# Optimization experiments

Measured on AMD Instinct MI355X. Metric: run time of the kernel, lower is better.

The kernel has to match this reference:

```python
import jax, jax.numpy as jnp
import numpy as np

N_NODES = 80000
N_EDGES = 1280000
N_FEAT = 4
HIDDEN = 64
N_CLASSES = 2
N_GRAPHS = 64
BN_EPS = 1e-5


def setup_inputs() -> dict:
    key = jax.random.key(0)
    ks = jax.random.split(key, 16)
    x = jax.random.normal(ks[0], (N_NODES, N_FEAT), dtype=jnp.float32)
    edge_index = jax.random.randint(ks[1], (2, N_EDGES), 0, N_NODES, dtype=jnp.int64)
    batch = jnp.sort(jax.random.randint(ks[2], (N_NODES,), 0, N_GRAPHS, dtype=jnp.int64))

    def lin_w(k, fan_in, fan_out):
        bound = 1.0 / np.sqrt(fan_in)
        return jax.random.uniform(k, (fan_in, fan_out), jnp.float32, -bound, bound)

    inp = {
        "x": x, "edge_index": edge_index, "batch": batch,
        # BatchNorm1d (eval mode: running stats)
        "bn_gamma": jnp.ones((N_FEAT,), jnp.float32),
        "bn_beta": jnp.zeros((N_FEAT,), jnp.float32),
        "bn_mean": jnp.zeros((N_FEAT,), jnp.float32),
        "bn_var": jnp.ones((N_FEAT,), jnp.float32),
        # GraphConv layers: out = agg @ W_rel + b_rel + x @ W_root
        "W1_rel": lin_w(ks[3], N_FEAT, HIDDEN), "b1_rel": jnp.zeros((HIDDEN,), jnp.float32),
        "W1_root": lin_w(ks[4], N_FEAT, HIDDEN),
        "W2_rel": lin_w(ks[5], HIDDEN, HIDDEN), "b2_rel": jnp.zeros((HIDDEN,), jnp.float32),
        "W2_root": lin_w(ks[6], HIDDEN, HIDDEN),
        "W3_rel": lin_w(ks[7], HIDDEN, HIDDEN), "b3_rel": jnp.zeros((HIDDEN,), jnp.float32),
        "W3_root": lin_w(ks[8], HIDDEN, HIDDEN),
        "lin_W": lin_w(ks[9], HIDDEN, N_CLASSES),
        "lin_b": jnp.zeros((N_CLASSES,), jnp.float32),
    }
    return inp


def _graph_conv(x, src, dst, W_rel, b_rel, W_root):
    # PyG GraphConv: x_i' = W_root x_i + W_rel * sum_{j in N(i)} x_j + b_rel
    agg = jax.ops.segment_sum(x[src], dst, num_segments=N_NODES)  # [N, C_in]
    return agg @ W_rel + b_rel + x @ W_root


def reference(x, edge_index, batch,
              bn_gamma, bn_beta, bn_mean, bn_var,
              W1_rel, b1_rel, W1_root,
              W2_rel, b2_rel, W2_root,
              W3_rel, b3_rel, W3_root,
              lin_W, lin_b):
    src, dst = edge_index[0], edge_index[1]
    # BatchNorm1d, eval mode (running stats); dropout is a no-op in eval.
    h = (x - bn_mean) * (bn_gamma * jax.lax.rsqrt(bn_var + BN_EPS)) + bn_beta
    h = jax.nn.relu(_graph_conv(h, src, dst, W1_rel, b1_rel, W1_root))
    h = jax.nn.relu(_graph_conv(h, src, dst, W2_rel, b2_rel, W2_root))
    h = _graph_conv(h, src, dst, W3_rel, b3_rel, W3_root)
    # global mean pool over graphs
    sums = jax.ops.segment_sum(h, batch, num_segments=N_GRAPHS)        # [G, H]
    cnts = jax.ops.segment_sum(jnp.ones((h.shape[0],), h.dtype), batch,
                               num_segments=N_GRAPHS)                  # [G]
    pooled = sums / jnp.maximum(cnts, 1.0)[:, None]
    return pooled @ lin_W + lin_b  # [G, num_classes]
```

## Files before the change

kernel.cpp:

```cpp
#include <hip/hip_runtime.h>
#include <hip/hip_bf16.h>

#define N_NODES 80000
#define N_EDGES 1280000
#define N_FEAT 4
#define HIDDEN 64
#define N_GRAPHS 64
#define BN_EPS 1e-5f

#define NBUCK 313
#define BCAP 8000

typedef unsigned short ushort_t;
typedef __attribute__((ext_vector_type(8))) short bf16x8;
typedef __attribute__((ext_vector_type(4))) float f32x4;

__device__ __forceinline__ float bf2f(ushort_t v) {
    return __uint_as_float(((unsigned)v) << 16);
}
__device__ __forceinline__ ushort_t f2bf(float f) {
    unsigned u = __float_as_uint(f);
    u += 0x7FFFu + ((u >> 16) & 1u);
    return (ushort_t)(u >> 16);
}

__global__ void wprep_kernel(const float* __restrict__ W2_rel,
                             const float* __restrict__ W2_root,
                             const float* __restrict__ W3_rel,
                             const float* __restrict__ W3_root,
                             ushort_t* __restrict__ WcatT2,
                             ushort_t* __restrict__ WcatT3,
                             int* __restrict__ bcursor,
                             float* __restrict__ pool,
                             float* __restrict__ cnt) {
    int i = blockIdx.x * blockDim.x + threadIdx.x;
    int which = i >= 64 * 128;
    int j = i & (64 * 128 - 1);
    int n = j >> 7, k = j & 127;
    const float* Wr = which ? W3_rel : W2_rel;
    const float* Wo = which ? W3_root : W2_root;
    ushort_t* Wc = which ? WcatT3 : WcatT2;
    float w = (k < 64) ? Wr[k * 64 + n] : Wo[(k - 64) * 64 + n];
    Wc[j] = f2bf(w);
    if (i < 4096) pool[i] = 0.f;
    else if (i < 4160) cnt[i - 4096] = 0.f;
    else if (i < 4160 + NBUCK) bcursor[i - 4160] = 0;
}

__global__ __launch_bounds__(256) void bucket_kernel(
        const int* __restrict__ src, const int* __restrict__ dst,
        unsigned* __restrict__ pairs, int* __restrict__ bcursor) {
    __shared__ int hist[NBUCK];
    __shared__ int base[NBUCK];
    for (int i = threadIdx.x; i < NBUCK; i += 256) hist[i] = 0;
    __syncthreads();
    int d[16], r[16];
#pragma unroll
    for (int g = 0; g < 4; ++g) {
        int e = blockIdx.x * 4096 + g * 1024 + threadIdx.x * 4;
        if (e + 4 <= N_EDGES) {
            int4 dd = *(const int4*)&dst[e];
            d[g * 4 + 0] = dd.x; d[g * 4 + 1] = dd.y;
            d[g * 4 + 2] = dd.z; d[g * 4 + 3] = dd.w;
            r[g * 4 + 0] = atomicAdd(&hist[dd.x >> 8], 1);
            r[g * 4 + 1] = atomicAdd(&hist[dd.y >> 8], 1);
            r[g * 4 + 2] = atomicAdd(&hist[dd.z >> 8], 1);
            r[g * 4 + 3] = atomicAdd(&hist[dd.w >> 8], 1);
        } else {
            d[g * 4] = -1;
        }
    }
    __syncthreads();
    for (int i = threadIdx.x; i < NBUCK; i += 256) {
        int c = hist[i];
        base[i] = c ? atomicAdd(&bcursor[i], c) : 0;
    }
    __syncthreads();
#pragma unroll
    for (int g = 0; g < 4; ++g) {
        int e = blockIdx.x * 4096 + g * 1024 + threadIdx.x * 4;
        if (e + 4 <= N_EDGES) {
            int4 ss = *(const int4*)&src[e];
            int sv[4] = {ss.x, ss.y, ss.z, ss.w};
#pragma unroll
            for (int k = 0; k < 4; ++k) {
                int dk = d[g * 4 + k];
                int b = dk >> 8;
                int pos = base[b] + r[g * 4 + k];
                if (pos < BCAP)
                    pairs[(size_t)b * BCAP + pos] =
                        (unsigned)sv[k] | (((unsigned)dk & 255u) << 17);
            }
        }
    }
}

__global__ __launch_bounds__(256) void csr_build_kernel(
        const unsigned* __restrict__ pairs, const int* __restrict__ bcursor,
        int* __restrict__ rowstart, int* __restrict__ csr) {
    __shared__ int degl[256];
    __shared__ int pref[256];
    __shared__ int curs[256];
    const int b = blockIdx.x;
    const int t = threadIdx.x;
    int partial = 0;
    for (int i = t; i < b; i += 256) partial += min(bcursor[i], BCAP);
    pref[t] = partial;
    __syncthreads();
    for (int off = 128; off > 0; off >>= 1) {
        if (t < off) pref[t] += pref[t + off];
        __syncthreads();
    }
    const int base = pref[0];
    const int cntb = min(bcursor[b], BCAP);
    __syncthreads();
    degl[t] = 0;
    __syncthreads();
    const unsigned* pb = pairs + (size_t)b * BCAP;
    for (int i = t * 4; i < cntb; i += 1024) {
        if (i + 4 <= cntb) {
            uint4 p4 = *(const uint4*)&pb[i];
            atomicAdd(&degl[p4.x >> 17], 1);
            atomicAdd(&degl[p4.y >> 17], 1);
            atomicAdd(&degl[p4.z >> 17], 1);
            atomicAdd(&degl[p4.w >> 17], 1);
        } else {
            for (int k = i; k < cntb; ++k) atomicAdd(&degl[pb[k] >> 17], 1);
        }
    }
    __syncthreads();
    int v = degl[t];
    pref[t] = v;
    __syncthreads();
    for (int off = 1; off < 256; off <<= 1) {
        int u = (t >= off) ? pref[t - off] : 0;
        __syncthreads();
        pref[t] += u;
        __syncthreads();
    }
    int excl = pref[t] - v;
    int node = b * 256 + t;
    if (node < N_NODES) rowstart[node] = base + excl;
    if (b == NBUCK - 1 && t == 255) rowstart[N_NODES] = base + cntb;
    curs[t] = excl;
    __syncthreads();
    for (int i = t * 4; i < cntb; i += 1024) {
        if (i + 4 <= cntb) {
            uint4 p4 = *(const uint4*)&pb[i];
            unsigned pv[4] = {p4.x, p4.y, p4.z, p4.w};
#pragma unroll
            for (int k = 0; k < 4; ++k) {
                int pos = atomicAdd(&curs[pv[k] >> 17], 1);
                csr[base + pos] = (int)(pv[k] & 0x1FFFFu);
            }
        } else {
            for (int k = i; k < cntb; ++k) {
                unsigned p = pb[k];
                int pos = atomicAdd(&curs[p >> 17], 1);
                csr[base + pos] = (int)(p & 0x1FFFFu);
            }
        }
    }
}

__global__ __launch_bounds__(256) void layer1_kernel(
        const float* __restrict__ x, ushort_t* __restrict__ h1,
        const int* __restrict__ rowstart, const int* __restrict__ csr,
        const float* __restrict__ Wrel, const float* __restrict__ Wroot,
        const float* __restrict__ b,
        const float* __restrict__ gamma, const float* __restrict__ beta,
        const float* __restrict__ mean, const float* __restrict__ var) {
    const int lane = threadIdx.x & 63;
    const int wid = threadIdx.x >> 6;
    float scale[4], shift[4];
#pragma unroll
    for (int k = 0; k < 4; ++k) {
        float sc = gamma[k] * rsqrtf(var[k] + BN_EPS);
        scale[k] = sc;
        shift[k] = beta[k] - mean[k] * sc;
    }
    float wrel2[4], wroot2[4];
    float crel = 0.f, croot = 0.f;
#pragma unroll
    for (int k = 0; k < 4; ++k) {
        float wr = Wrel[k * 64 + lane], wo = Wroot[k * 64 + lane];
        wrel2[k] = scale[k] * wr;  crel += shift[k] * wr;
        wroot2[k] = scale[k] * wo; croot += shift[k] * wo;
    }
    const float bj = b[lane] + croot;
    const int slot = lane >> 2;
    const int f = lane & 3;
    const int node = __builtin_amdgcn_readfirstlane(blockIdx.x * 4 + wid);
    const int e0 = rowstart[node], e1 = rowstart[node + 1];
    const float deg = (float)(e1 - e0);
    const int last = e1 - 1;
    float part = 0.f;
    for (int e = e0; e < e1; e += 16) {
        int s = csr[min(e + slot, last)];
        float v = x[s * 4 + f];
        part += (e + slot < e1) ? v : 0.f;
    }
    part += __shfl_xor(part, 4);
    part += __shfl_xor(part, 8);
    part += __shfl_xor(part, 16);
    part += __shfl_xor(part, 32);
    float a0 = __shfl(part, 0), a1 = __shfl(part, 1);
    float a2 = __shfl(part, 2), a3 = __shfl(part, 3);
    float x0 = x[node * 4 + 0], x1 = x[node * 4 + 1];
    float x2 = x[node * 4 + 2], x3 = x[node * 4 + 3];
    float out = bj + deg * crel
              + a0 * wrel2[0] + a1 * wrel2[1] + a2 * wrel2[2] + a3 * wrel2[3]
              + x0 * wroot2[0] + x1 * wroot2[1] + x2 * wroot2[2] + x3 * wroot2[3];
    h1[(size_t)node * 64 + lane] = f2bf(fmaxf(out, 0.f));
}

__global__ __launch_bounds__(256) void gather_kernel(
        const ushort_t* __restrict__ hin, ushort_t* __restrict__ Gagg,
        const int* __restrict__ rowstart, const int* __restrict__ csr) {
    const int lane = threadIdx.x & 63;
    const int l4 = lane & 15;
    const int q = lane >> 4;
    const int node = __builtin_amdgcn_readfirstlane(blockIdx.x * 4 + (threadIdx.x >> 6));
    const int e0 = rowstart[node], e1 = rowstart[node + 1];
    float ax[4], ay[4], az[4], aw[4];
#pragma unroll
    for (int j = 0; j < 4; ++j) { ax[j] = 0.f; ay[j] = 0.f; az[j] = 0.f; aw[j] = 0.f; }
    int e = e0;
    for (; e + 16 <= e1; e += 16) {
        int idx = csr[e + (lane & 15)];
#pragma unroll
        for (int j = 0; j < 4; ++j) {
            int s = __shfl(idx, 4 * j + q);
            uint2 rp = *(const uint2*)&hin[(size_t)s * 64 + 4 * l4];
            ax[j] += __uint_as_float(rp.x << 16);
            ay[j] += __uint_as_float(rp.x & 0xFFFF0000u);
            az[j] += __uint_as_float(rp.y << 16);
            aw[j] += __uint_as_float(rp.y & 0xFFFF0000u);
        }
    }
    if (e < e1) {
        const int rem = e1 - e;
        const int last = e1 - 1;
        int idx = csr[min(e + (lane & 15), last)];
#pragma unroll
        for (int j = 0; j < 4; ++j) {
            int slot = 4 * j + q;
            int s = __shfl(idx, slot);
            uint2 rp = *(const uint2*)&hin[(size_t)s * 64 + 4 * l4];
            bool ok = slot < rem;
            ax[j] += ok ? __uint_as_float(rp.x << 16) : 0.f;
            ay[j] += ok ? __uint_as_float(rp.x & 0xFFFF0000u) : 0.f;
            az[j] += ok ? __uint_as_float(rp.y << 16) : 0.f;
            aw[j] += ok ? __uint_as_float(rp.y & 0xFFFF0000u) : 0.f;
        }
    }
    float fx = (ax[0] + ax[1]) + (ax[2] + ax[3]);
    float fy = (ay[0] + ay[1]) + (ay[2] + ay[3]);
    float fz = (az[0] + az[1]) + (az[2] + az[3]);
    float fw = (aw[0] + aw[1]) + (aw[2] + aw[3]);
    fx += __shfl_xor(fx, 16); fx += __shfl_xor(fx, 32);
    fy += __shfl_xor(fy, 16); fy += __shfl_xor(fy, 32);
    fz += __shfl_xor(fz, 16); fz += __shfl_xor(fz, 32);
    fw += __shfl_xor(fw, 16); fw += __shfl_xor(fw, 32);
    if (q == 0) {
        uint2 ap;
        ap.x = (unsigned)f2bf(fx) | ((unsigned)f2bf(fy) << 16);
        ap.y = (unsigned)f2bf(fz) | ((unsigned)f2bf(fw) << 16);
        ((uint2*)(Gagg + (size_t)node * 64))[l4] = ap;
    }
}

__global__ __launch_bounds__(256) void gemm_kernel(
        const ushort_t* __restrict__ Gagg, const ushort_t* __restrict__ hin,
        ushort_t* __restrict__ hout,
        const ushort_t* __restrict__ WcatT, const float* __restrict__ b,
        int relu) {
    const int lane = threadIdx.x & 63;
    const int col = lane & 15;
    const int grp = lane >> 4;

    bf16x8 bf[4][4];
#pragma unroll
    for (int kt = 0; kt < 4; ++kt)
#pragma unroll
        for (int nt = 0; nt < 4; ++nt)
            bf[kt][nt] = *(const bf16x8*)&WcatT[(nt * 16 + col) * 128 + kt * 32 + grp * 8];

    float bj[4];
#pragma unroll
    for (int nt = 0; nt < 4; ++nt) bj[nt] = b[nt * 16 + col];

    const int tile = blockIdx.x * 4 + (threadIdx.x >> 6);
    if (tile >= N_NODES / 16) return;
    const int node0 = tile * 16;

    const ushort_t* ga = Gagg + (size_t)(node0 + col) * 64 + grp * 8;
    const ushort_t* ha = hin + (size_t)(node0 + col) * 64 + grp * 8;
    f32x4 acc0 = {0.f, 0.f, 0.f, 0.f};
    f32x4 acc1 = {0.f, 0.f, 0.f, 0.f};
    f32x4 acc2 = {0.f, 0.f, 0.f, 0.f};
    f32x4 acc3 = {0.f, 0.f, 0.f, 0.f};
#pragma unroll
    for (int kt = 0; kt < 4; ++kt) {
        bf16x8 a = (kt < 2) ? *(const bf16x8*)(ga + kt * 32)
                            : *(const bf16x8*)(ha + (kt - 2) * 32);
        acc0 = __builtin_amdgcn_mfma_f32_16x16x32_bf16(a, bf[kt][0], acc0, 0, 0, 0);
        acc1 = __builtin_amdgcn_mfma_f32_16x16x32_bf16(a, bf[kt][1], acc1, 0, 0, 0);
        acc2 = __builtin_amdgcn_mfma_f32_16x16x32_bf16(a, bf[kt][2], acc2, 0, 0, 0);
        acc3 = __builtin_amdgcn_mfma_f32_16x16x32_bf16(a, bf[kt][3], acc3, 0, 0, 0);
    }

#pragma unroll
    for (int nt = 0; nt < 4; ++nt) {
        f32x4 acc = (nt == 0) ? acc0 : (nt == 1) ? acc1 : (nt == 2) ? acc2 : acc3;
        const int c = nt * 16 + col;
#pragma unroll
        for (int r = 0; r < 4; ++r) {
            int row = grp * 4 + r;
            float v = acc[r] + bj[nt];
            if (relu) v = fmaxf(v, 0.f);
            hout[(size_t)(node0 + row) * 64 + c] = f2bf(v);
        }
    }
}

__global__ void pool_kernel(const ushort_t* __restrict__ h3, const int* __restrict__ batch,
                            float* __restrict__ pool, float* __restrict__ cnt) {
    const int lane = threadIdx.x & 63;
    const int gw = (blockIdx.x * blockDim.x + threadIdx.x) >> 6;
    const int nW = (gridDim.x * blockDim.x) >> 6;
    const int chunk = (N_NODES + nW - 1) / nW;
    int n0 = gw * chunk;
    int n1 = n0 + chunk; if (n1 > N_NODES) n1 = N_NODES;
    if (n0 >= N_NODES) return;
    float acc = 0.f;
    int cur = batch[n0];
    int cl = 0;
#define POOL_FLUSH() do { atomicAdd(&pool[cur * 64 + lane], acc); \
        if (lane == 0) atomicAdd(&cnt[cur], (float)cl); acc = 0.f; cl = 0; } while (0)
    int n = n0;
    for (; n + 8 <= n1; n += 8) {
        float v0 = bf2f(h3[(size_t)(n + 0) * 64 + lane]);
        float v1 = bf2f(h3[(size_t)(n + 1) * 64 + lane]);
        float v2 = bf2f(h3[(size_t)(n + 2) * 64 + lane]);
        float v3 = bf2f(h3[(size_t)(n + 3) * 64 + lane]);
        float v4 = bf2f(h3[(size_t)(n + 4) * 64 + lane]);
        float v5 = bf2f(h3[(size_t)(n + 5) * 64 + lane]);
        float v6 = bf2f(h3[(size_t)(n + 6) * 64 + lane]);
        float v7 = bf2f(h3[(size_t)(n + 7) * 64 + lane]);
        int g0 = batch[n + 0], g1 = batch[n + 1], g2 = batch[n + 2], g3 = batch[n + 3];
        int g4 = batch[n + 4], g5 = batch[n + 5], g6 = batch[n + 6], g7 = batch[n + 7];
        if (g0 != cur) { POOL_FLUSH(); cur = g0; } acc += v0; cl++;
        if (g1 != cur) { POOL_FLUSH(); cur = g1; } acc += v1; cl++;
        if (g2 != cur) { POOL_FLUSH(); cur = g2; } acc += v2; cl++;
        if (g3 != cur) { POOL_FLUSH(); cur = g3; } acc += v3; cl++;
        if (g4 != cur) { POOL_FLUSH(); cur = g4; } acc += v4; cl++;
        if (g5 != cur) { POOL_FLUSH(); cur = g5; } acc += v5; cl++;
        if (g6 != cur) { POOL_FLUSH(); cur = g6; } acc += v6; cl++;
        if (g7 != cur) { POOL_FLUSH(); cur = g7; } acc += v7; cl++;
    }
    for (; n < n1; ++n) {
        int g = batch[n];
        if (g != cur) { POOL_FLUSH(); cur = g; }
        acc += bf2f(h3[(size_t)n * 64 + lane]);
        cl++;
    }
    atomicAdd(&pool[cur * 64 + lane], acc);
    if (lane == 0) atomicAdd(&cnt[cur], (float)cl);
#undef POOL_FLUSH
}

__global__ void head_kernel(const float* __restrict__ pool, const float* __restrict__ cnt,
                            const float* __restrict__ linW, const float* __restrict__ linb,
                            float* __restrict__ out) {
    int g = threadIdx.x >> 1;
    int c = threadIdx.x & 1;
    if (g < N_GRAPHS) {
        float inv = 1.0f / fmaxf(cnt[g], 1.0f);
        float acc = linb[c];
        for (int j = 0; j < 64; ++j) acc += pool[g * 64 + j] * inv * linW[j * 2 + c];
        out[g * 2 + c] = acc;
    }
}

extern "C" void kernel_launch(void* const* d_in, const int* in_sizes, int n_in,
                              void* d_out, int out_size, void* d_ws, size_t ws_size,
                              hipStream_t stream) {
    const float* x = (const float*)d_in[0];
    const int* edge_index = (const int*)d_in[1];
    const int* batch = (const int*)d_in[2];
    const float* bn_gamma = (const float*)d_in[3];
    const float* bn_beta = (const float*)d_in[4];
    const float* bn_mean = (const float*)d_in[5];
    const float* bn_var = (const float*)d_in[6];
    const float* W1_rel = (const float*)d_in[7];
    const float* b1_rel = (const float*)d_in[8];
    const float* W1_root = (const float*)d_in[9];
    const float* W2_rel = (const float*)d_in[10];
    const float* b2_rel = (const float*)d_in[11];
    const float* W2_root = (const float*)d_in[12];
    const float* W3_rel = (const float*)d_in[13];
    const float* b3_rel = (const float*)d_in[14];
    const float* W3_root = (const float*)d_in[15];
    const float* lin_W = (const float*)d_in[16];
    const float* lin_b = (const float*)d_in[17];
    float* out = (float*)d_out;

    const int* e_src = edge_index;
    const int* e_dst = edge_index + N_EDGES;

    ushort_t* h1 = (ushort_t*)d_ws;
    ushort_t* h2 = h1 + 5120000;
    float* pool = (float*)(h2 + 5120000);
    float* cnt = pool + 4096;
    int* bcursor = (int*)(cnt + 64);
    int* rowstart = bcursor + 640;
    int* csr = rowstart + 80016;
    ushort_t* WcatT2 = (ushort_t*)(csr + 1280000);
    ushort_t* WcatT3 = WcatT2 + 8192;
    ushort_t* Gagg = (ushort_t*)(WcatT3 + 8192 + 16);
    unsigned* pairs = (unsigned*)h1;
    ushort_t* h3 = h1;

    wprep_kernel<<<64, 256, 0, stream>>>(W2_rel, W2_root, W3_rel, W3_root,
                                         WcatT2, WcatT3, bcursor, pool, cnt);

    bucket_kernel<<<(N_EDGES + 4095) / 4096, 256, 0, stream>>>(
        e_src, e_dst, pairs, bcursor);
    csr_build_kernel<<<NBUCK, 256, 0, stream>>>(pairs, bcursor, rowstart, csr);

    layer1_kernel<<<N_NODES / 4, 256, 0, stream>>>(x, h1, rowstart, csr, W1_rel, W1_root,
                                                   b1_rel, bn_gamma, bn_beta, bn_mean, bn_var);

    gather_kernel<<<N_NODES / 4, 256, 0, stream>>>(h1, Gagg, rowstart, csr);
    gemm_kernel<<<N_NODES / 64, 256, 0, stream>>>(Gagg, h1, h2, WcatT2, b2_rel, 1);

    gather_kernel<<<N_NODES / 4, 256, 0, stream>>>(h2, Gagg, rowstart, csr);
    gemm_kernel<<<N_NODES / 64, 256, 0, stream>>>(Gagg, h2, h3, WcatT3, b3_rel, 0);

    pool_kernel<<<256, 256, 0, stream>>>(h3, batch, pool, cnt);
    head_kernel<<<1, 128, 0, stream>>>(pool, cnt, lin_W, lin_b, out);
}
```

Baseline: 173.3 us.

## Fuse neighbor gather with MFMA GEMM per layer and make layer1 grid-stride

Merges the gather and GEMM kernels into one kernel per GraphConv layer. Each block aggregates 16 nodes into a shared-memory tile, then each of its four waves computes one 16-column slice with MFMA, so the Gagg intermediate no longer makes a round trip through global memory. Layer1 becomes a persistent grid-stride kernel with 1024-thread blocks and loses its masked tail handling. In exchange, each block waits on a barrier behind its slowest node, and fewer gather waves run per tile.

```diff
diff --git a/kernel.cpp b/kernel.cpp
--- a/kernel.cpp
+++ b/kernel.cpp
@@ -163,7 +163,7 @@
     }
 }
 
-__global__ __launch_bounds__(256) void layer1_kernel(
+__global__ __launch_bounds__(1024) void layer1_kernel(
         const float* __restrict__ x, ushort_t* __restrict__ h1,
         const int* __restrict__ rowstart, const int* __restrict__ csr,
         const float* __restrict__ Wrel, const float* __restrict__ Wroot,
@@ -188,139 +188,121 @@
         wroot2[k] = scale[k] * wo; croot += shift[k] * wo;
     }
     const float bj = b[lane] + croot;
-    const int slot = lane >> 2;
+    const int sub = lane >> 2;
     const int f = lane & 3;
-    const int node = __builtin_amdgcn_readfirstlane(blockIdx.x * 4 + wid);
-    const int e0 = rowstart[node], e1 = rowstart[node + 1];
-    const float deg = (float)(e1 - e0);
-    const int last = e1 - 1;
-    float part = 0.f;
-    for (int e = e0; e < e1; e += 16) {
-        int s = csr[min(e + slot, last)];
-        float v = x[s * 4 + f];
-        part += (e + slot < e1) ? v : 0.f;
-    }
-    part += __shfl_xor(part, 4);
-    part += __shfl_xor(part, 8);
-    part += __shfl_xor(part, 16);
-    part += __shfl_xor(part, 32);
-    float a0 = __shfl(part, 0), a1 = __shfl(part, 1);
-    float a2 = __shfl(part, 2), a3 = __shfl(part, 3);
-    float x0 = x[node * 4 + 0], x1 = x[node * 4 + 1];
-    float x2 = x[node * 4 + 2], x3 = x[node * 4 + 3];
-    float out = bj + deg * crel
-              + a0 * wrel2[0] + a1 * wrel2[1] + a2 * wrel2[2] + a3 * wrel2[3]
-              + x0 * wroot2[0] + x1 * wroot2[1] + x2 * wroot2[2] + x3 * wroot2[3];
-    h1[(size_t)node * 64 + lane] = f2bf(fmaxf(out, 0.f));
-}
-
-__global__ __launch_bounds__(256) void gather_kernel(
-        const ushort_t* __restrict__ hin, ushort_t* __restrict__ Gagg,
-        const int* __restrict__ rowstart, const int* __restrict__ csr) {
+    const int nW = gridDim.x * 16;
+    for (int n0 = blockIdx.x * 16 + wid; n0 < N_NODES; n0 += nW) {
+        const int node = __builtin_amdgcn_readfirstlane(n0);
+        const int e0 = rowstart[node], e1 = rowstart[node + 1];
+        const float deg = (float)(e1 - e0);
+        float part = 0.f;
+        for (int e = e0 + sub; e < e1; e += 16) {
+            int s = csr[e];
+            part += x[s * 4 + f];
+        }
+        part += __shfl_xor(part, 4);
+        part += __shfl_xor(part, 8);
+        part += __shfl_xor(part, 16);
+        part += __shfl_xor(part, 32);
+        float a0 = __shfl(part, 0), a1 = __shfl(part, 1);
+        float a2 = __shfl(part, 2), a3 = __shfl(part, 3);
+        float x0 = x[node * 4 + 0], x1 = x[node * 4 + 1];
+        float x2 = x[node * 4 + 2], x3 = x[node * 4 + 3];
+        float out = bj + deg * crel
+                  + a0 * wrel2[0] + a1 * wrel2[1] + a2 * wrel2[2] + a3 * wrel2[3]
+                  + x0 * wroot2[0] + x1 * wroot2[1] + x2 * wroot2[2] + x3 * wroot2[3];
+        h1[(size_t)node * 64 + lane] = f2bf(fmaxf(out, 0.f));
+    }
+}
+
+__global__ __launch_bounds__(256) void fused_layer_kernel(
+        const ushort_t* __restrict__ hin, ushort_t* __restrict__ hout,
+        const int* __restrict__ rowstart, const int* __restrict__ csr,
+        const ushort_t* __restrict__ WcatT, const float* __restrict__ b,
+        int relu) {
+    __shared__ ushort_t As[16][72];
     const int lane = threadIdx.x & 63;
+    const int wid = threadIdx.x >> 6;
     const int l4 = lane & 15;
     const int q = lane >> 4;
-    const int node = __builtin_amdgcn_readfirstlane(blockIdx.x * 4 + (threadIdx.x >> 6));
-    const int e0 = rowstart[node], e1 = rowstart[node + 1];
-    float ax[4], ay[4], az[4], aw[4];
-#pragma unroll
-    for (int j = 0; j < 4; ++j) { ax[j] = 0.f; ay[j] = 0.f; az[j] = 0.f; aw[j] = 0.f; }
-    int e = e0;
-    for (; e + 16 <= e1; e += 16) {
-        int idx = csr[e + (lane & 15)];
-#pragma unroll
-        for (int j = 0; j < 4; ++j) {
-            int s = __shfl(idx, 4 * j + q);
-            uint2 rp = *(const uint2*)&hin[(size_t)s * 64 + 4 * l4];
-            ax[j] += __uint_as_float(rp.x << 16);
-            ay[j] += __uint_as_float(rp.x & 0xFFFF0000u);
-            az[j] += __uint_as_float(rp.y << 16);
-            aw[j] += __uint_as_float(rp.y & 0xFFFF0000u);
-        }
-    }
-    if (e < e1) {
-        const int rem = e1 - e;
-        const int last = e1 - 1;
-        int idx = csr[min(e + (lane & 15), last)];
-#pragma unroll
-        for (int j = 0; j < 4; ++j) {
-            int slot = 4 * j + q;
-            int s = __shfl(idx, slot);
-            uint2 rp = *(const uint2*)&hin[(size_t)s * 64 + 4 * l4];
-            bool ok = slot < rem;
-            ax[j] += ok ? __uint_as_float(rp.x << 16) : 0.f;
-            ay[j] += ok ? __uint_as_float(rp.x & 0xFFFF0000u) : 0.f;
-            az[j] += ok ? __uint_as_float(rp.y << 16) : 0.f;
-            aw[j] += ok ? __uint_as_float(rp.y & 0xFFFF0000u) : 0.f;
-        }
-    }
-    float fx = (ax[0] + ax[1]) + (ax[2] + ax[3]);
-    float fy = (ay[0] + ay[1]) + (ay[2] + ay[3]);
-    float fz = (az[0] + az[1]) + (az[2] + az[3]);
-    float fw = (aw[0] + aw[1]) + (aw[2] + aw[3]);
-    fx += __shfl_xor(fx, 16); fx += __shfl_xor(fx, 32);
-    fy += __shfl_xor(fy, 16); fy += __shfl_xor(fy, 32);
-    fz += __shfl_xor(fz, 16); fz += __shfl_xor(fz, 32);
-    fw += __shfl_xor(fw, 16); fw += __shfl_xor(fw, 32);
-    if (q == 0) {
-        uint2 ap;
-        ap.x = (unsigned)f2bf(fx) | ((unsigned)f2bf(fy) << 16);
-        ap.y = (unsigned)f2bf(fz) | ((unsigned)f2bf(fw) << 16);
-        ((uint2*)(Gagg + (size_t)node * 64))[l4] = ap;
-    }
-}
-
-__global__ __launch_bounds__(256) void gemm_kernel(
-        const ushort_t* __restrict__ Gagg, const ushort_t* __restrict__ hin,
-        ushort_t* __restrict__ hout,
-        const ushort_t* __restrict__ WcatT, const float* __restrict__ b,
-        int relu) {
-    const int lane = threadIdx.x & 63;
+    const int node0 = blockIdx.x * 16;
+
+    for (int i = 0; i < 4; ++i) {
+        const int row = wid * 4 + i;
+        const int node = __builtin_amdgcn_readfirstlane(node0 + row);
+        const int e0 = rowstart[node], e1 = rowstart[node + 1];
+        float ax[4], ay[4], az[4], aw[4];
+#pragma unroll
+        for (int j = 0; j < 4; ++j) { ax[j] = 0.f; ay[j] = 0.f; az[j] = 0.f; aw[j] = 0.f; }
+        int e = e0;
+        for (; e + 16 <= e1; e += 16) {
+            int idx = csr[e + (lane & 15)];
+#pragma unroll
+            for (int j = 0; j < 4; ++j) {
+                int s = __shfl(idx, 4 * j + q);
+                uint2 rp = *(const uint2*)&hin[(size_t)s * 64 + 4 * l4];
+                ax[j] += __uint_as_float(rp.x << 16);
+                ay[j] += __uint_as_float(rp.x & 0xFFFF0000u);
+                az[j] += __uint_as_float(rp.y << 16);
+                aw[j] += __uint_as_float(rp.y & 0xFFFF0000u);
+            }
+        }
+        if (e < e1) {
+            const int rem = e1 - e;
+            const int last = e1 - 1;
+            int idx = csr[min(e + (lane & 15), last)];
+#pragma unroll
+            for (int j = 0; j < 4; ++j) {
+                int slot = 4 * j + q;
+                int s = __shfl(idx, slot);
+                uint2 rp = *(const uint2*)&hin[(size_t)s * 64 + 4 * l4];
+                bool ok = slot < rem;
+                ax[j] += ok ? __uint_as_float(rp.x << 16) : 0.f;
+                ay[j] += ok ? __uint_as_float(rp.x & 0xFFFF0000u) : 0.f;
+                az[j] += ok ? __uint_as_float(rp.y << 16) : 0.f;
+                aw[j] += ok ? __uint_as_float(rp.y & 0xFFFF0000u) : 0.f;
+            }
+        }
+        float fx = (ax[0] + ax[1]) + (ax[2] + ax[3]);
+        float fy = (ay[0] + ay[1]) + (ay[2] + ay[3]);
+        float fz = (az[0] + az[1]) + (az[2] + az[3]);
+        float fw = (aw[0] + aw[1]) + (aw[2] + aw[3]);
+        fx += __shfl_xor(fx, 16); fx += __shfl_xor(fx, 32);
+        fy += __shfl_xor(fy, 16); fy += __shfl_xor(fy, 32);
+        fz += __shfl_xor(fz, 16); fz += __shfl_xor(fz, 32);
+        fw += __shfl_xor(fw, 16); fw += __shfl_xor(fw, 32);
+        if (lane < 16) {
+            uint2 ap;
+            ap.x = (unsigned)f2bf(fx) | ((unsigned)f2bf(fy) << 16);
+            ap.y = (unsigned)f2bf(fz) | ((unsigned)f2bf(fw) << 16);
+            *(uint2*)&As[row][l4 * 4] = ap;
+        }
+    }
+    __syncthreads();
+
     const int col = lane & 15;
     const int grp = lane >> 4;
-
-    bf16x8 bf[4][4];
+    bf16x8 bf[4];
 #pragma unroll
     for (int kt = 0; kt < 4; ++kt)
-#pragma unroll
-        for (int nt = 0; nt < 4; ++nt)
-            bf[kt][nt] = *(const bf16x8*)&WcatT[(nt * 16 + col) * 128 + kt * 32 + grp * 8];
-
-    float bj[4];
-#pragma unroll
-    for (int nt = 0; nt < 4; ++nt) bj[nt] = b[nt * 16 + col];
-
-    const int tile = blockIdx.x * 4 + (threadIdx.x >> 6);
-    if (tile >= N_NODES / 16) return;
-    const int node0 = tile * 16;
-
-    const ushort_t* ga = Gagg + (size_t)(node0 + col) * 64 + grp * 8;
+        bf[kt] = *(const bf16x8*)&WcatT[(wid * 16 + col) * 128 + kt * 32 + grp * 8];
+    const float bj = b[wid * 16 + col];
+
     const ushort_t* ha = hin + (size_t)(node0 + col) * 64 + grp * 8;
-    f32x4 acc0 = {0.f, 0.f, 0.f, 0.f};
-    f32x4 acc1 = {0.f, 0.f, 0.f, 0.f};
-    f32x4 acc2 = {0.f, 0.f, 0.f, 0.f};
-    f32x4 acc3 = {0.f, 0.f, 0.f, 0.f};
+    f32x4 acc = {0.f, 0.f, 0.f, 0.f};
 #pragma unroll
     for (int kt = 0; kt < 4; ++kt) {
-        bf16x8 a = (kt < 2) ? *(const bf16x8*)(ga + kt * 32)
+        bf16x8 a = (kt < 2) ? *(const bf16x8*)&As[col][kt * 32 + grp * 8]
                             : *(const bf16x8*)(ha + (kt - 2) * 32);
-        acc0 = __builtin_amdgcn_mfma_f32_16x16x32_bf16(a, bf[kt][0], acc0, 0, 0, 0);
-        acc1 = __builtin_amdgcn_mfma_f32_16x16x32_bf16(a, bf[kt][1], acc1, 0, 0, 0);
-        acc2 = __builtin_amdgcn_mfma_f32_16x16x32_bf16(a, bf[kt][2], acc2, 0, 0, 0);
-        acc3 = __builtin_amdgcn_mfma_f32_16x16x32_bf16(a, bf[kt][3], acc3, 0, 0, 0);
-    }
-
-#pragma unroll
-    for (int nt = 0; nt < 4; ++nt) {
-        f32x4 acc = (nt == 0) ? acc0 : (nt == 1) ? acc1 : (nt == 2) ? acc2 : acc3;
-        const int c = nt * 16 + col;
-#pragma unroll
-        for (int r = 0; r < 4; ++r) {
-            int row = grp * 4 + r;
-            float v = acc[r] + bj[nt];
-            if (relu) v = fmaxf(v, 0.f);
-            hout[(size_t)(node0 + row) * 64 + c] = f2bf(v);
-        }
+        acc = __builtin_amdgcn_mfma_f32_16x16x32_bf16(a, bf[kt], acc, 0, 0, 0);
+    }
+    const int c = wid * 16 + col;
+#pragma unroll
+    for (int r = 0; r < 4; ++r) {
+        int row = grp * 4 + r;
+        float v = acc[r] + bj;
+        if (relu) v = fmaxf(v, 0.f);
+        hout[(size_t)(node0 + row) * 64 + c] = f2bf(v);
     }
 }
 
@@ -418,7 +400,6 @@
     int* csr = rowstart + 80016;
     ushort_t* WcatT2 = (ushort_t*)(csr + 1280000);
     ushort_t* WcatT3 = WcatT2 + 8192;
-    ushort_t* Gagg = (ushort_t*)(WcatT3 + 8192 + 16);
     unsigned* pairs = (unsigned*)h1;
     ushort_t* h3 = h1;
 
@@ -429,14 +410,13 @@
         e_src, e_dst, pairs, bcursor);
     csr_build_kernel<<<NBUCK, 256, 0, stream>>>(pairs, bcursor, rowstart, csr);
 
-    layer1_kernel<<<N_NODES / 4, 256, 0, stream>>>(x, h1, rowstart, csr, W1_rel, W1_root,
-                                                   b1_rel, bn_gamma, bn_beta, bn_mean, bn_var);
-
-    gather_kernel<<<N_NODES / 4, 256, 0, stream>>>(h1, Gagg, rowstart, csr);
-    gemm_kernel<<<N_NODES / 64, 256, 0, stream>>>(Gagg, h1, h2, WcatT2, b2_rel, 1);
-
-    gather_kernel<<<N_NODES / 4, 256, 0, stream>>>(h2, Gagg, rowstart, csr);
-    gemm_kernel<<<N_NODES / 64, 256, 0, stream>>>(Gagg, h2, h3, WcatT3, b3_rel, 0);
+    layer1_kernel<<<512, 1024, 0, stream>>>(x, h1, rowstart, csr, W1_rel, W1_root,
+                                            b1_rel, bn_gamma, bn_beta, bn_mean, bn_var);
+
+    fused_layer_kernel<<<N_NODES / 16, 256, 0, stream>>>(
+        h1, h2, rowstart, csr, WcatT2, b2_rel, 1);
+    fused_layer_kernel<<<N_NODES / 16, 256, 0, stream>>>(
+        h2, h3, rowstart, csr, WcatT3, b3_rel, 0);
 
     pool_kernel<<<256, 256, 0, stream>>>(h3, batch, pool, cnt);
     head_kernel<<<1, 128, 0, stream>>>(pool, cnt, lin_W, lin_b, out);
```

After: 162.3 us, median of 2. 6.3% less time.
